# Kernel optimization log

Measured on AMD Instinct MI355X. Metric: run time of the kernel, lower is better.

## Reference

```python
import jax, jax.numpy as jnp
import numpy as np

EPS = 1e-5  # LayerNorm eps (torch default)
K_NN = 16   # matches init kwarg k


def _knn_idx(pos, k):
    # pos: (B,N,3) -> (B,N,k) indices of k nearest points (sorted by distance,
    # includes self at slot 0), matching pytorch3d knn_points(return_sorted=True).
    sq = jnp.sum(pos * pos, axis=-1)                                   # (B,N)
    d2 = sq[:, :, None] + sq[:, None, :] - 2.0 * jnp.einsum('bnd,bmd->bnm', pos, pos)
    _, idx = jax.lax.top_k(-d2, k)                                     # ascending distance
    return idx


def _gather(feats, idx):
    # feats: (B,N,C), idx: (B,N,K) -> (B,N,K,C)
    return jax.vmap(lambda f, i: f[i])(feats, idx)


def _ln(x, g, b):
    mu = jnp.mean(x, axis=-1, keepdims=True)
    var = jnp.mean((x - mu) ** 2, axis=-1, keepdims=True)
    return (x - mu) * jax.lax.rsqrt(var + EPS) * g + b


def setup_inputs() -> dict:
    key = jax.random.key(0)
    B, N, D, H = 2, 4096, 128, 12
    ks = jax.random.split(key, 16)
    s = 0.05
    f32 = jnp.float32
    return {
        'x': jax.random.normal(ks[0], (B, N, D), f32),
        'pos': jax.random.normal(ks[1], (B, N, 3), f32),
        # linear projections (bias=False)
        'w_q': jax.random.normal(ks[2], (D, D), f32) * s,
        'w_k': jax.random.normal(ks[3], (D, D), f32) * s,
        'w_v': jax.random.normal(ks[4], (D, D), f32) * s,
        # pos_mlp: Linear(3,H) -> LN(H) -> ReLU -> Linear(H,D)
        'pos_w1': jax.random.normal(ks[5], (H, 3), f32) * s,
        'pos_b1': jnp.zeros((H,), f32),
        'pos_g': jnp.ones((H,), f32),
        'pos_beta': jnp.zeros((H,), f32),
        'pos_w2': jax.random.normal(ks[6], (D, H), f32) * s,
        'pos_b2': jnp.zeros((D,), f32),
        # attn_mlp: Linear(D,D) -> LN(D) -> ReLU -> Linear(D,D)
        'attn_w1': jax.random.normal(ks[7], (D, D), f32) * s,
        'attn_b1': jnp.zeros((D,), f32),
        'attn_g': jnp.ones((D,), f32),
        'attn_beta': jnp.zeros((D,), f32),
        'attn_w2': jax.random.normal(ks[8], (D, D), f32) * s,
        'attn_b2': jnp.zeros((D,), f32),
    }


def reference(x, pos, w_q, w_k, w_v,
              pos_w1, pos_b1, pos_g, pos_beta, pos_w2, pos_b2,
              attn_w1, attn_b1, attn_g, attn_beta, attn_w2, attn_b2):
    idx = _knn_idx(pos, K_NN)                        # (B,N,K)
    q = x @ w_q.T                                    # (B,N,D)
    kf = _gather(x @ w_k.T, idx)                     # (B,N,K,D)
    vf = _gather(x @ w_v.T, idx)                     # (B,N,K,D)
    pos_rel = pos[:, :, None, :] - _gather(pos, idx)  # (B,N,K,3)
    # pos_mlp
    pe = _ln(pos_rel @ pos_w1.T + pos_b1, pos_g, pos_beta)
    pe = jax.nn.relu(pe) @ pos_w2.T + pos_b2         # (B,N,K,D)
    # attn_mlp on (q - k + pos_enc)
    w = q[:, :, None, :] - kf + pe
    w = _ln(w @ attn_w1.T + attn_b1, attn_g, attn_beta)
    w = jax.nn.relu(w) @ attn_w2.T + attn_b2         # (B,N,K,D)
    attn = jax.nn.softmax(w, axis=2)                 # softmax over neighbor dim
    return jnp.einsum('bnkd,bnkd->bnd', attn, vf + pe)
```

## Files before the change

### kernel.cpp

```cpp
#include <hip/hip_runtime.h>
#include <hip/hip_bf16.h>
#include <math.h>

#define BATCH 2
#define NPTS 4096
#define DIM 128
#define HID 12
#define KNN 16
#define NSLOT 24
#define BCAP 192
#define BCT 64
#define PTQ 4

#define FOLD_BLOCKS 128
#define M1_BLOCKS 32
#define PRE_BLOCKS (FOLD_BLOCKS + M1_BLOCKS + 4)
#define KNN_BLOCKS (BATCH * NPTS / 4)

typedef __attribute__((ext_vector_type(8))) short short8;
typedef __attribute__((ext_vector_type(4))) float f32x4;

__device__ __forceinline__ short f2b(float f) {
  unsigned u = __float_as_uint(f);
  unsigned r = (u + 0x7fffu + ((u >> 16) & 1u)) >> 16;
  return (short)r;
}
__device__ __forceinline__ float b2f(short h) {
  return __uint_as_float(((unsigned)(unsigned short)h) << 16);
}

#define BITONIC64(v, vi)                                                     \
  {                                                                          \
    _Pragma("unroll") for (int k_ = 2; k_ <= 64; k_ <<= 1) {                 \
      _Pragma("unroll") for (int j_ = k_ >> 1; j_ >= 1; j_ >>= 1) {          \
        const float ov_ = __shfl_xor((v), j_);                               \
        const int oi_ = __shfl_xor((vi), j_);                                \
        const bool up_ = ((lane & k_) == 0);                                 \
        const bool lowpos_ = ((lane & j_) == 0);                             \
        const bool keep_min_ = (lowpos_ == up_);                             \
        const bool lt_ = (ov_ < (v)) || (ov_ == (v) && oi_ < (vi));          \
        const bool take_ = keep_min_ ? lt_ : !lt_;                           \
        if (take_) { (v) = ov_; (vi) = oi_; }                                \
      }                                                                      \
    }                                                                        \
  }

__device__ void knn_body(int bid, const float* __restrict__ pos,
                         int* __restrict__ knn_out) {
  __shared__ float bd_s[4][BCAP];
  __shared__ int bi_s[4][BCAP];

  const int t = threadIdx.x;
  const int w = t >> 6;
  const int lane = t & 63;
  const int n = (bid << 2) + w;
  const int b = n >> 12;
  const int qn = n & (NPTS - 1);

  float* bdl = &bd_s[w][0];
  int* bil = &bi_s[w][0];

  const float* pb = pos + b * NPTS * 3;
  const float qx = pb[qn * 3 + 0];
  const float qy = pb[qn * 3 + 1];
  const float qz = pb[qn * 3 + 2];

  const bool is_slot = (lane < NSLOT);
  float vald, thr;
  int validx;
  int bcount = 0;

  {
    const float2* pp = (const float2*)(pb + lane * 6);
    const float2 u0 = pp[0], u1 = pp[1], u2 = pp[2];
    float dx = qx - u0.x, dy = qy - u0.y, dz = qz - u1.x;
    float v = fmaf(dx, dx, fmaf(dy, dy, dz * dz));
    int vi = lane * 2;
    dx = qx - u1.y; dy = qy - u2.x; dz = qz - u2.y;
    const float d2b = fmaf(dx, dx, fmaf(dy, dy, dz * dz));

    BITONIC64(v, vi)
    vald = is_slot ? v : __builtin_inff();
    validx = is_slot ? vi : 0x7fffffff;
    const float v15 = __shfl(v, 15);
    thr = v15 + v15 * 1e-5f;

    const unsigned long long m = __ballot(d2b < thr);
    if (m) {
      const unsigned lt = __builtin_amdgcn_mbcnt_hi(
          (unsigned)(m >> 32), __builtin_amdgcn_mbcnt_lo((unsigned)m, 0u));
      if (d2b < thr) { bdl[lt] = d2b; bil[lt] = 2 * lane + 1; }
      bcount = (int)__builtin_popcountll(m);
    }
  }

  const float2* pp = (const float2*)(pb + 384 + lane * 6);
  float2 A0 = pp[0], A1 = pp[1], A2 = pp[2];
  pp = (const float2*)(pb + 768 + lane * 6);
  float2 B0 = pp[0], B1 = pp[1], B2 = pp[2];

#pragma unroll 1
  for (int it = 1; it < NPTS / 128; ++it) {
    const float2 c0 = A0, c1v = A1, c2 = A2;
    A0 = B0; A1 = B1; A2 = B2;
    if (it + 2 < NPTS / 128) {
      pp = (const float2*)(pb + (it + 2) * 384 + lane * 6);
      B0 = pp[0]; B1 = pp[1]; B2 = pp[2];
    }
    float dx = qx - c0.x, dy = qy - c0.y, dz = qz - c1v.x;
    const float e2a = fmaf(dx, dx, fmaf(dy, dy, dz * dz));
    dx = qx - c1v.y; dy = qy - c2.x; dz = qz - c2.y;
    const float e2b = fmaf(dx, dx, fmaf(dy, dy, dz * dz));

    if (bcount >= BCT) {
#pragma unroll 1
      while (bcount > 0) {
        const int take = bcount < 40 ? bcount : 40;
        float mv = __builtin_inff();
        int mi = 0x7fffffff;
        if (lane < NSLOT) { mv = vald; mi = validx; }
        else if (lane - NSLOT < take) {
          mv = bdl[bcount - take + lane - NSLOT];
          mi = bil[bcount - take + lane - NSLOT];
        }
        BITONIC64(mv, mi)
        if (is_slot) { vald = mv; validx = mi; }
        bcount -= take;
      }
      const float v15 = __shfl(vald, 15);
      thr = v15 + v15 * 1e-5f;
    }

    {
      const unsigned long long m = __ballot(e2a < thr);
      if (m) {
        const unsigned lt = __builtin_amdgcn_mbcnt_hi(
            (unsigned)(m >> 32), __builtin_amdgcn_mbcnt_lo((unsigned)m, 0u));
        if (e2a < thr) { bdl[bcount + lt] = e2a; bil[bcount + lt] = it * 128 + 2 * lane; }
        bcount += (int)__builtin_popcountll(m);
      }
    }
    {
      const unsigned long long m = __ballot(e2b < thr);
      if (m) {
        const unsigned lt = __builtin_amdgcn_mbcnt_hi(
            (unsigned)(m >> 32), __builtin_amdgcn_mbcnt_lo((unsigned)m, 0u));
        if (e2b < thr) { bdl[bcount + lt] = e2b; bil[bcount + lt] = it * 128 + 2 * lane + 1; }
        bcount += (int)__builtin_popcountll(m);
      }
    }
  }

#pragma unroll 1
  while (bcount > 0) {
    const int take = bcount < 40 ? bcount : 40;
    float mv = __builtin_inff();
    int mi = 0x7fffffff;
    if (lane < NSLOT) { mv = vald; mi = validx; }
    else if (lane - NSLOT < take) {
      mv = bdl[bcount - take + lane - NSLOT];
      mi = bil[bcount - take + lane - NSLOT];
    }
    BITONIC64(mv, mi)
    if (is_slot) { vald = mv; validx = mi; }
    bcount -= take;
  }

  double d2e = 1e300;
  if (is_slot) {
    const double ex = (double)qx - (double)pb[validx * 3 + 0];
    const double ey = (double)qy - (double)pb[validx * 3 + 1];
    const double ez = (double)qz - (double)pb[validx * 3 + 2];
    d2e = ex * ex + ey * ey + ez * ez;
  }
  int rank = 0;
#pragma unroll 1
  for (int j = 0; j < NSLOT; ++j) {
    const double dj = __shfl(d2e, j);
    const int ij = __shfl(validx, j);
    if (dj < d2e || (dj == d2e && ij < validx)) ++rank;
  }
  if (is_slot && rank < KNN) knn_out[((b << 12) + qn) * KNN + rank] = validx;
}

__device__ void fold_body(int bid, const float* __restrict__ aw1,
                          const float* __restrict__ wq, const float* __restrict__ wk,
                          short* __restrict__ WqaHi, short* __restrict__ WqaLo,
                          short* __restrict__ WkaHi, short* __restrict__ WkaLo) {
  const float* w = (bid < 64) ? wq : wk;
  short* oh = (bid < 64) ? WqaHi : WkaHi;
  short* ol = (bid < 64) ? WqaLo : WkaLo;
  const int row = ((bid & 63) << 1) + (threadIdx.x >> 7);
  const int i = threadIdx.x & 127;
  float acc = 0.f;
  for (int j = 0; j < 128; ++j) acc = fmaf(aw1[row * 128 + j], w[j * 128 + i], acc);
  const short h = f2b(acc);
  oh[row * 128 + i] = h;
  ol[row * 128 + i] = f2b(acc - b2f(h));
}

__device__ void m1_body(int bid, const float* __restrict__ aw1,
                        const float* __restrict__ pw2, const float* __restrict__ pb2,
                        const float* __restrict__ ab1,
                        short* __restrict__ M1b, float* __restrict__ c1) {
  const int t = threadIdx.x;
  const int wid = t >> 6, lane = t & 63;
  const int o = bid * 4 + wid;
  const float a0 = aw1[o * 128 + lane];
  const float a1 = aw1[o * 128 + 64 + lane];

  float s = fmaf(a0, pb2[lane], a1 * pb2[64 + lane]);
#pragma unroll
  for (int off = 1; off < 64; off <<= 1) s += __shfl_xor(s, off);
  if (lane == 0) c1[o] = ab1[o] + s;

#pragma unroll
  for (int k = 0; k < HID; ++k) {
    float p = fmaf(a0, pw2[lane * HID + k], a1 * pw2[(64 + lane) * HID + k]);
#pragma unroll
    for (int off = 1; off < 64; off <<= 1) p += __shfl_xor(p, off);
    if (lane == 0) M1b[o * 32 + k] = f2b(p);
  }
  if (lane >= HID && lane < 32) M1b[o * 32 + lane] = 0;
}

__device__ void pw2b_body(const float* __restrict__ pw2, short* __restrict__ pw2b) {
  const int t = threadIdx.x;
  for (int i = t; i < 128 * 32; i += 256) {
    const int o = i >> 5, k = i & 31;
    pw2b[i] = (k < HID) ? f2b(pw2[o * HID + k]) : (short)0;
  }
}
__device__ void aw2b_body(int half, const float* __restrict__ aw2,
                          short* __restrict__ aw2b) {
  const int base = half * 8192;
  for (int i = threadIdx.x; i < 8192; i += 256) aw2b[base + i] = f2b(aw2[base + i]);
}
__device__ void wv_body(const float* __restrict__ wv, short* __restrict__ WvHi,
                        short* __restrict__ WvLo) {
  for (int i = threadIdx.x; i < 128 * 128; i += 256) {
    const float v = wv[i];
    const short h = f2b(v);
    WvHi[i] = h;
    WvLo[i] = f2b(v - b2f(h));
  }
}

__global__ __launch_bounds__(256) void knn_prep_kernel(
    const float* __restrict__ pos, int* __restrict__ knn_out,
    const float* __restrict__ aw1, const float* __restrict__ wq,
    const float* __restrict__ wk,
    short* __restrict__ WqaHi, short* __restrict__ WqaLo,
    short* __restrict__ WkaHi, short* __restrict__ WkaLo,
    const float* __restrict__ pw2, const float* __restrict__ pb2,
    const float* __restrict__ ab1, const float* __restrict__ aw2,
    const float* __restrict__ wv,
    short* __restrict__ M1b, short* __restrict__ pw2b, short* __restrict__ aw2b,
    float* __restrict__ c1, short* __restrict__ WvHi, short* __restrict__ WvLo) {
  const int bid = blockIdx.x;
  if (bid < FOLD_BLOCKS) {
    fold_body(bid, aw1, wq, wk, WqaHi, WqaLo, WkaHi, WkaLo);
  } else if (bid < FOLD_BLOCKS + M1_BLOCKS) {
    m1_body(bid - FOLD_BLOCKS, aw1, pw2, pb2, ab1, M1b, c1);
  } else if (bid == FOLD_BLOCKS + M1_BLOCKS) {
    pw2b_body(pw2, pw2b);
  } else if (bid <= FOLD_BLOCKS + M1_BLOCKS + 2) {
    aw2b_body(bid - (FOLD_BLOCKS + M1_BLOCKS + 1), aw2, aw2b);
  } else if (bid == FOLD_BLOCKS + M1_BLOCKS + 3) {
    wv_body(wv, WvHi, WvLo);
  } else {
    knn_body(bid - PRE_BLOCKS, pos, knn_out);
  }
}

__global__ __launch_bounds__(256) void proj_mfma_kernel(
    const float* __restrict__ x,
    const short* __restrict__ WqaHi, const short* __restrict__ WqaLo,
    const short* __restrict__ WkaHi, const short* __restrict__ WkaLo,
    const short* __restrict__ WvHi, const short* __restrict__ WvLo,
    short* __restrict__ QAb, short* __restrict__ KAb, short* __restrict__ Vpb) {
  const int t = threadIdx.x;
  const int wid = t >> 6, lane = t & 63;
  const int r16 = lane & 15, g4 = lane >> 4;
  const int rowbase = blockIdx.x * 32 + (wid >> 1) * 16;
  const int ch = wid & 1;

  short8 ahi[4], alo[4];
#pragma unroll
  for (int ks = 0; ks < 4; ++ks) {
    const float* xp = x + (rowbase + r16) * DIM + ks * 32 + g4 * 8;
#pragma unroll
    for (int e = 0; e < 8; ++e) {
      const float v = xp[e];
      const short h = f2b(v);
      ahi[ks][e] = h;
      alo[ks][e] = f2b(v - b2f(h));
    }
  }

  const f32x4 zero4 = {0.f, 0.f, 0.f, 0.f};
  const short* WH[3] = {WqaHi, WkaHi, WvHi};
  const short* WL[3] = {WqaLo, WkaLo, WvLo};
  short* OUT[3] = {QAb, KAb, Vpb};
#pragma unroll
  for (int mi = 0; mi < 3; ++mi) {
    const short* wh = WH[mi];
    const short* wl = WL[mi];
    short* o = OUT[mi];
#pragma unroll
    for (int q = 0; q < 4; ++q) {
      const int col = (ch * 4 + q) * 16 + r16;
      f32x4 a = zero4;
#pragma unroll
      for (int ks = 0; ks < 4; ++ks) {
        const short8 bh = *(const short8*)(wh + col * DIM + ks * 32 + g4 * 8);
        const short8 bl = *(const short8*)(wl + col * DIM + ks * 32 + g4 * 8);
        a = __builtin_amdgcn_mfma_f32_16x16x32_bf16(ahi[ks], bh, a, 0, 0, 0);
        a = __builtin_amdgcn_mfma_f32_16x16x32_bf16(alo[ks], bh, a, 0, 0, 0);
        a = __builtin_amdgcn_mfma_f32_16x16x32_bf16(ahi[ks], bl, a, 0, 0, 0);
      }
#pragma unroll
      for (int reg = 0; reg < 4; ++reg)
        o[(rowbase + g4 * 4 + reg) * DIM + (ch * 4 + q) * 16 + r16] = f2b(a[reg]);
    }
  }
}

__global__ __launch_bounds__(256) void pt_wave_kernel(
    const float* __restrict__ pos, const int* __restrict__ knn_in,
    const short* __restrict__ QAb, const short* __restrict__ KAb,
    const short* __restrict__ Vpb,
    const float* __restrict__ pw1, const float* __restrict__ pb1,
    const float* __restrict__ pg, const float* __restrict__ pbeta,
    const float* __restrict__ pb2,
    const float* __restrict__ ag, const float* __restrict__ abeta,
    const float* __restrict__ ab2, const float* __restrict__ c1,
    const short* __restrict__ M1b, const short* __restrict__ pw2b,
    const short* __restrict__ aw2b,
    float* __restrict__ out) {
  __shared__ __align__(16) short z_s[2048];
  __shared__ float red_s[2][4][16];
  __shared__ short hr_s[16][HID];

  const int t = threadIdx.x;
  const int wid = t >> 6;
  const int lane = t & 63;
  const int r16 = lane & 15;
  const int g4 = lane >> 4;
  const f32x4 zero4 = {0.f, 0.f, 0.f, 0.f};

  short8 BM[2], BP[2], BW[2][4];
  float c1v[2], agv[2], abtv[2], ab2v[2], pb2v[2];
#pragma unroll
  for (int q = 0; q < 2; ++q) {
    const int o = (wid * 2 + q) * 16 + r16;
    const int boff = o * 32 + g4 * 8;
    BM[q] = *(const short8*)(M1b + boff);
    BP[q] = *(const short8*)(pw2b + boff);
#pragma unroll
    for (int ks = 0; ks < 4; ++ks)
      BW[q][ks] = *(const short8*)(aw2b + o * DIM + ks * 32 + g4 * 8);
    c1v[q] = c1[o];
    agv[q] = ag[o];
    abtv[q] = abeta[o];
    ab2v[q] = ab2[o];
    pb2v[q] = pb2[o];
  }

#pragma unroll 1
  for (int qi = 0; qi < PTQ; ++qi) {
    const int n = blockIdx.x * PTQ + qi;
    const int b = n >> 12;

    int myidx = 0;
    if (lane < KNN) myidx = knn_in[n * KNN + lane];
    int jC[4];
#pragma unroll
    for (int reg = 0; reg < 4; ++reg) jC[reg] = __shfl(myidx, g4 * 4 + reg);

    const bool pm = (wid == 0) && (lane < 16);

    float rx = 0.f, ry = 0.f, rz = 0.f;
    if (pm) {
      const int jg = b * NPTS + myidx;
      rx = pos[n * 3 + 0] - pos[jg * 3 + 0];
      ry = pos[n * 3 + 1] - pos[jg * 3 + 1];
      rz = pos[n * 3 + 2] - pos[jg * 3 + 2];
    }

    float qa_[2], kav[2][4], vv[2][4];
#pragma unroll
    for (int q = 0; q < 2; ++q) {
      const int o = (wid * 2 + q) * 16 + r16;
      qa_[q] = b2f(QAb[n * DIM + o]);
#pragma unroll
      for (int reg = 0; reg < 4; ++reg) {
        const int row = b * NPTS + jC[reg];
        kav[q][reg] = b2f(KAb[row * DIM + o]);
        vv[q][reg] = b2f(Vpb[row * DIM + o]);
      }
    }

    if (pm) {
      float hr[HID];
      float mu = 0.f;
#pragma unroll
      for (int hh = 0; hh < HID; ++hh) {
        const float v = pb1[hh] + rx * pw1[hh * 3 + 0] + ry * pw1[hh * 3 + 1] +
                        rz * pw1[hh * 3 + 2];
        hr[hh] = v;
        mu += v;
      }
      mu *= (1.f / HID);
      float var = 0.f;
#pragma unroll
      for (int hh = 0; hh < HID; ++hh) { const float d = hr[hh] - mu; var = fmaf(d, d, var); }
      const float rsn = rsqrtf(var * (1.f / HID) + 1e-5f);
#pragma unroll
      for (int hh = 0; hh < HID; ++hh)
        hr_s[lane][hh] = f2b(fmaxf(fmaf((hr[hh] - mu) * rsn, pg[hh], pbeta[hh]), 0.f));
    }
    __syncthreads();

    short8 a1 = {0, 0, 0, 0, 0, 0, 0, 0};
    if (g4 == 0) {
#pragma unroll
      for (int e = 0; e < 8; ++e) a1[e] = hr_s[r16][e];
    } else if (g4 == 1) {
#pragma unroll
      for (int e = 0; e < 4; ++e) a1[e] = hr_s[r16][8 + e];
    }

    f32x4 accw[2], accp[2];
#pragma unroll
    for (int q = 0; q < 2; ++q) {
      accw[q] = __builtin_amdgcn_mfma_f32_16x16x32_bf16(a1, BM[q], zero4, 0, 0, 0);
      accp[q] = __builtin_amdgcn_mfma_f32_16x16x32_bf16(a1, BP[q], zero4, 0, 0, 0);
    }

    float w1v[2][4];
#pragma unroll
    for (int q = 0; q < 2; ++q) {
      const float base = qa_[q] + c1v[q];
#pragma unroll
      for (int reg = 0; reg < 4; ++reg)
        w1v[q][reg] = accw[q][reg] + base - kav[q][reg];
    }

    {
      float ps[4], pq2[4];
#pragma unroll
      for (int reg = 0; reg < 4; ++reg) {
        ps[reg] = w1v[0][reg] + w1v[1][reg];
        pq2[reg] = fmaf(w1v[0][reg], w1v[0][reg], w1v[1][reg] * w1v[1][reg]);
      }
#pragma unroll
      for (int reg = 0; reg < 4; ++reg) {
#pragma unroll
        for (int off = 1; off <= 8; off <<= 1) {
          ps[reg] += __shfl_xor(ps[reg], off);
          pq2[reg] += __shfl_xor(pq2[reg], off);
        }
      }
      if (r16 == 0) {
#pragma unroll
        for (int reg = 0; reg < 4; ++reg) {
          red_s[0][wid][g4 * 4 + reg] = ps[reg];
          red_s[1][wid][g4 * 4 + reg] = pq2[reg];
        }
      }
    }
    __syncthreads();
    float mu[4], rs[4];
#pragma unroll
    for (int reg = 0; reg < 4; ++reg) {
      const int rr = g4 * 4 + reg;
      const float s = red_s[0][0][rr] + red_s[0][1][rr] + red_s[0][2][rr] + red_s[0][3][rr];
      const float q2 = red_s[1][0][rr] + red_s[1][1][rr] + red_s[1][2][rr] + red_s[1][3][rr];
      mu[reg] = s * (1.f / 128.f);
      const float var = q2 * (1.f / 128.f) - mu[reg] * mu[reg];
      rs[reg] = rsqrtf(var + 1e-5f);
    }

    {
      char* zb = (char*)z_s;
#pragma unroll
      for (int q = 0; q < 2; ++q) {
        const int o = (wid * 2 + q) * 16 + r16;
#pragma unroll
        for (int reg = 0; reg < 4; ++reg) {
          const int rr = g4 * 4 + reg;
          const float zv = fmaxf(fmaf((w1v[q][reg] - mu[reg]) * rs[reg], agv[q], abtv[q]), 0.f);
          unsigned byte = (unsigned)(rr * 256 + o * 2);
          byte ^= ((unsigned)(rr & 7) << 4) ^ ((unsigned)(rr & 8) << 2);
          *(short*)(zb + byte) = f2b(zv);
        }
      }
    }
    __syncthreads();

    short8 a2[4];
    {
      const char* zb = (const char*)z_s;
#pragma unroll
      for (int ks = 0; ks < 4; ++ks) {
        unsigned byte = (unsigned)(r16 * 256 + ks * 64 + g4 * 16);
        byte ^= ((unsigned)(r16 & 7) << 4) ^ ((unsigned)(r16 & 8) << 2);
        a2[ks] = *(const short8*)(zb + byte);
      }
    }

    f32x4 acc2[2] = {zero4, zero4};
#pragma unroll
    for (int q = 0; q < 2; ++q) {
#pragma unroll
      for (int ks = 0; ks < 4; ++ks)
        acc2[q] = __builtin_amdgcn_mfma_f32_16x16x32_bf16(a2[ks], BW[q][ks], acc2[q], 0, 0, 0);
    }

    float ew[2][4], inv[2];
#pragma unroll
    for (int q = 0; q < 2; ++q) {
#pragma unroll
      for (int reg = 0; reg < 4; ++reg) ew[q][reg] = acc2[q][reg] + ab2v[q];
      float m = fmaxf(fmaxf(ew[q][0], ew[q][1]), fmaxf(ew[q][2], ew[q][3]));
      m = fmaxf(m, __shfl_xor(m, 16));
      m = fmaxf(m, __shfl_xor(m, 32));
      float s = 0.f;
#pragma unroll
      for (int reg = 0; reg < 4; ++reg) { ew[q][reg] = __expf(ew[q][reg] - m); s += ew[q][reg]; }
      s += __shfl_xor(s, 16);
      s += __shfl_xor(s, 32);
      inv[q] = 1.f / s;
    }

    float o_acc[2];
#pragma unroll
    for (int q = 0; q < 2; ++q) {
      float acc = 0.f;
#pragma unroll
      for (int reg = 0; reg < 4; ++reg)
        acc = fmaf(ew[q][reg] * inv[q], vv[q][reg] + accp[q][reg] + pb2v[q], acc);
      acc += __shfl_xor(acc, 16);
      acc += __shfl_xor(acc, 32);
      o_acc[q] = acc;
    }
    if (g4 < 2) out[n * DIM + (wid * 2 + g4) * 16 + r16] = o_acc[g4];
  }
}

extern "C" void kernel_launch(void* const* d_in, const int* in_sizes, int n_in,
                              void* d_out, int out_size, void* d_ws, size_t ws_size,
                              hipStream_t stream) {
  const float* x   = (const float*)d_in[0];
  const float* pos = (const float*)d_in[1];
  const float* wq  = (const float*)d_in[2];
  const float* wk  = (const float*)d_in[3];
  const float* wv  = (const float*)d_in[4];
  const float* pw1 = (const float*)d_in[5];
  const float* pb1 = (const float*)d_in[6];
  const float* pg  = (const float*)d_in[7];
  const float* pbt = (const float*)d_in[8];
  const float* pw2 = (const float*)d_in[9];
  const float* pb2 = (const float*)d_in[10];
  const float* aw1 = (const float*)d_in[11];
  const float* ab1 = (const float*)d_in[12];
  const float* ag  = (const float*)d_in[13];
  const float* abt = (const float*)d_in[14];
  const float* aw2 = (const float*)d_in[15];
  const float* ab2 = (const float*)d_in[16];
  float* out = (float*)d_out;

  char* ws = (char*)d_ws;
  int*   knn   = (int*)ws;
  short* WqaHi = (short*)(ws + 512u * 1024u);
  short* WqaLo = (short*)(ws + 544u * 1024u);
  short* WkaHi = (short*)(ws + 576u * 1024u);
  short* WkaLo = (short*)(ws + 608u * 1024u);
  short* M1b   = (short*)(ws + 640u * 1024u);
  short* pw2b  = (short*)(ws + 648u * 1024u);
  short* aw2b  = (short*)(ws + 656u * 1024u);
  float* c1    = (float*)(ws + 688u * 1024u);
  short* WvHi  = (short*)(ws + 704u * 1024u);
  short* WvLo  = (short*)(ws + 736u * 1024u);
  short* QAb   = (short*)(ws + (1u << 20));
  short* KAb   = (short*)(ws + 4u * (1u << 20));
  short* Vpb   = (short*)(ws + 7u * (1u << 20));

  knn_prep_kernel<<<PRE_BLOCKS + KNN_BLOCKS, 256, 0, stream>>>(
      pos, knn, aw1, wq, wk, WqaHi, WqaLo, WkaHi, WkaLo, pw2, pb2, ab1, aw2, wv,
      M1b, pw2b, aw2b, c1, WvHi, WvLo);
  proj_mfma_kernel<<<BATCH * NPTS / 32, 256, 0, stream>>>(
      x, WqaHi, WqaLo, WkaHi, WkaLo, WvHi, WvLo, QAb, KAb, Vpb);
  pt_wave_kernel<<<BATCH * NPTS / PTQ, 256, 0, stream>>>(
      pos, knn, QAb, KAb, Vpb, pw1, pb1, pg, pbt, pb2, ag, abt, ab2, c1,
      M1b, pw2b, aw2b, out);
}
```

Before: 117.4 us.

## Regroup kernels so kNN overlaps projection, prefetch neighbor indices, double points per block

Moves the kNN search out of the weight-prep kernel into a fused launch with the MFMA projection. The prep kernel is now tiny, and the projection and kNN blocks share one grid so their work can overlap. In the attention kernel, each block now handles 8 points instead of 4, which spreads the per-block weight register loads over more points. The next point's neighbor indices are software-prefetched during the current iteration. Risks are fewer blocks in the attention grid and load imbalance between the mixed block types.

```diff
diff --git a/kernel.cpp b/kernel.cpp
--- a/kernel.cpp
+++ b/kernel.cpp
@@ -10,11 +10,12 @@
 #define NSLOT 24
 #define BCAP 192
 #define BCT 64
-#define PTQ 4
+#define PTQ 8
 
 #define FOLD_BLOCKS 128
 #define M1_BLOCKS 32
-#define PRE_BLOCKS (FOLD_BLOCKS + M1_BLOCKS + 4)
+#define PREP_BLOCKS (FOLD_BLOCKS + M1_BLOCKS + 4)
+#define PROJ_BLOCKS (BATCH * NPTS / 32)
 #define KNN_BLOCKS (BATCH * NPTS / 4)
 
 typedef __attribute__((ext_vector_type(8))) short short8;
@@ -246,8 +247,7 @@
   }
 }
 
-__global__ __launch_bounds__(256) void knn_prep_kernel(
-    const float* __restrict__ pos, int* __restrict__ knn_out,
+__global__ __launch_bounds__(256) void prep_kernel(
     const float* __restrict__ aw1, const float* __restrict__ wq,
     const float* __restrict__ wk,
     short* __restrict__ WqaHi, short* __restrict__ WqaLo,
@@ -266,23 +266,21 @@
     pw2b_body(pw2, pw2b);
   } else if (bid <= FOLD_BLOCKS + M1_BLOCKS + 2) {
     aw2b_body(bid - (FOLD_BLOCKS + M1_BLOCKS + 1), aw2, aw2b);
-  } else if (bid == FOLD_BLOCKS + M1_BLOCKS + 3) {
+  } else {
     wv_body(wv, WvHi, WvLo);
-  } else {
-    knn_body(bid - PRE_BLOCKS, pos, knn_out);
-  }
-}
-
-__global__ __launch_bounds__(256) void proj_mfma_kernel(
-    const float* __restrict__ x,
-    const short* __restrict__ WqaHi, const short* __restrict__ WqaLo,
-    const short* __restrict__ WkaHi, const short* __restrict__ WkaLo,
-    const short* __restrict__ WvHi, const short* __restrict__ WvLo,
-    short* __restrict__ QAb, short* __restrict__ KAb, short* __restrict__ Vpb) {
+  }
+}
+
+__device__ void proj_body(int bid, const float* __restrict__ x,
+                          const short* __restrict__ WqaHi, const short* __restrict__ WqaLo,
+                          const short* __restrict__ WkaHi, const short* __restrict__ WkaLo,
+                          const short* __restrict__ WvHi, const short* __restrict__ WvLo,
+                          short* __restrict__ QAb, short* __restrict__ KAb,
+                          short* __restrict__ Vpb) {
   const int t = threadIdx.x;
   const int wid = t >> 6, lane = t & 63;
   const int r16 = lane & 15, g4 = lane >> 4;
-  const int rowbase = blockIdx.x * 32 + (wid >> 1) * 16;
+  const int rowbase = bid * 32 + (wid >> 1) * 16;
   const int ch = wid & 1;
 
   short8 ahi[4], alo[4];
@@ -323,6 +321,21 @@
       for (int reg = 0; reg < 4; ++reg)
         o[(rowbase + g4 * 4 + reg) * DIM + (ch * 4 + q) * 16 + r16] = f2b(a[reg]);
     }
+  }
+}
+
+__global__ __launch_bounds__(256) void knn_proj_kernel(
+    const float* __restrict__ pos, int* __restrict__ knn_out,
+    const float* __restrict__ x,
+    const short* __restrict__ WqaHi, const short* __restrict__ WqaLo,
+    const short* __restrict__ WkaHi, const short* __restrict__ WkaLo,
+    const short* __restrict__ WvHi, const short* __restrict__ WvLo,
+    short* __restrict__ QAb, short* __restrict__ KAb, short* __restrict__ Vpb) {
+  const int bid = blockIdx.x;
+  if (bid < PROJ_BLOCKS) {
+    proj_body(bid, x, WqaHi, WqaLo, WkaHi, WkaLo, WvHi, WvLo, QAb, KAb, Vpb);
+  } else {
+    knn_body(bid - PROJ_BLOCKS, pos, knn_out);
   }
 }
 
@@ -367,13 +380,19 @@
     pb2v[q] = pb2[o];
   }
 
+  const int n0 = blockIdx.x * PTQ;
+  int curIdx = 0;
+  if (lane < KNN) curIdx = knn_in[n0 * KNN + lane];
+
 #pragma unroll 1
   for (int qi = 0; qi < PTQ; ++qi) {
-    const int n = blockIdx.x * PTQ + qi;
+    const int n = n0 + qi;
     const int b = n >> 12;
 
-    int myidx = 0;
-    if (lane < KNN) myidx = knn_in[n * KNN + lane];
+    int nxtIdx = 0;
+    if (qi + 1 < PTQ && lane < KNN) nxtIdx = knn_in[(n + 1) * KNN + lane];
+    const int myidx = curIdx;
+
     int jC[4];
 #pragma unroll
     for (int reg = 0; reg < 4; ++reg) jC[reg] = __shfl(myidx, g4 * 4 + reg);
@@ -546,6 +565,8 @@
       o_acc[q] = acc;
     }
     if (g4 < 2) out[n * DIM + (wid * 2 + g4) * 16 + r16] = o_acc[g4];
+
+    curIdx = nxtIdx;
   }
 }
 
@@ -587,11 +608,11 @@
   short* KAb   = (short*)(ws + 4u * (1u << 20));
   short* Vpb   = (short*)(ws + 7u * (1u << 20));
 
-  knn_prep_kernel<<<PRE_BLOCKS + KNN_BLOCKS, 256, 0, stream>>>(
-      pos, knn, aw1, wq, wk, WqaHi, WqaLo, WkaHi, WkaLo, pw2, pb2, ab1, aw2, wv,
+  prep_kernel<<<PREP_BLOCKS, 256, 0, stream>>>(
+      aw1, wq, wk, WqaHi, WqaLo, WkaHi, WkaLo, pw2, pb2, ab1, aw2, wv,
       M1b, pw2b, aw2b, c1, WvHi, WvLo);
-  proj_mfma_kernel<<<BATCH * NPTS / 32, 256, 0, stream>>>(
-      x, WqaHi, WqaLo, WkaHi, WkaLo, WvHi, WvLo, QAb, KAb, Vpb);
+  knn_proj_kernel<<<PROJ_BLOCKS + KNN_BLOCKS, 256, 0, stream>>>(
+      pos, knn, x, WqaHi, WqaLo, WkaHi, WkaLo, WvHi, WvLo, QAb, KAb, Vpb);
   pt_wave_kernel<<<BATCH * NPTS / PTQ, 256, 0, stream>>>(
       pos, knn, QAb, KAb, Vpb, pw1, pb1, pg, pbt, pb2, ag, abt, ab2, c1,
       M1b, pw2b, aw2b, out);
```

Result: slower. 124.8 us (+6.3%).
